# Kernel tuning notes

Hardware: AMD Instinct MI355X
Metric: run time of the kernel (lower is better)

Reference implementation:

```python
import jax, jax.numpy as jnp
import numpy as np

AZ = -999999.0  # ALMOST_ZERO_LOG_SCALE
N = 100000      # nodes
E = N - 1       # tree edges
D = 768         # input_dim
H = 256         # hidden_dim
C = 16          # num_classes


def setup_inputs() -> dict:
    key = jax.random.key(0)
    ks = jax.random.split(key, 14)
    scale = 0.02
    features = jax.random.normal(ks[0], (N, D), dtype=jnp.float32)
    # tree edges: child i (1..N-1) has parent sampled from [0, N)
    parent_idx = jax.random.randint(ks[1], (E,), 0, N, dtype=jnp.int32)
    child_idx = jnp.arange(1, N, dtype=jnp.int32)
    label_observed = jax.random.randint(ks[2], (N,), 0, 2, dtype=jnp.int32)
    true_labels = jax.random.randint(ks[3], (N,), 0, C, dtype=jnp.int32)
    # MLP feature extractor (num_layers=2, Linear+ReLU each, feature_extractor=True)
    W1 = jax.random.normal(ks[4], (D, H), dtype=jnp.float32) * scale
    b1 = jnp.zeros((H,), dtype=jnp.float32)
    W2 = jax.random.normal(ks[5], (H, H), dtype=jnp.float32) * scale
    b2 = jnp.zeros((H,), dtype=jnp.float32)
    # build_unary_potentials: Linear(H, C)
    Wu = jax.random.normal(ks[6], (H, C), dtype=jnp.float32) * scale
    bu = jnp.zeros((C,), dtype=jnp.float32)
    # build_edge_potentials: Linear(2H, C*C)
    We = jax.random.normal(ks[7], (2 * H, C * C), dtype=jnp.float32) * scale
    be = jnp.zeros((C * C,), dtype=jnp.float32)
    return {
        "features": features, "parent_idx": parent_idx, "child_idx": child_idx,
        "label_observed": label_observed, "true_labels": true_labels,
        "W1": W1, "b1": b1, "W2": W2, "b2": b2,
        "Wu": Wu, "bu": bu, "We": We, "be": be,
    }


def reference(features, parent_idx, child_idx, label_observed, true_labels,
              W1, b1, W2, b2, Wu, bu, We, be):
    obs = label_observed.astype(bool)
    # MLP feature extractor over all nodes at once (original loops per-node)
    h = jax.nn.relu(features @ W1 + b1)
    h = jax.nn.relu(h @ W2 + b2)                      # [N, H]
    # unary potentials; observed nodes get 0 at true label, AZ elsewhere
    unary_pred = h @ Wu + bu                          # [N, C]
    lbl = jnp.arange(C, dtype=true_labels.dtype)
    obs_unary = jnp.where(true_labels[:, None] == lbl[None, :], 0.0, AZ)
    unary = jnp.where(obs[:, None], obs_unary, unary_pred)  # [N, C]
    # edge potentials: Linear on concat(parent_hidden, child_hidden)
    hp = h[parent_idx]                                # [E, H]
    hc = h[child_idx]                                 # [E, H]
    ep = (jnp.concatenate([hp, hc], axis=1) @ We + be).reshape(E, C, C)
    pl = true_labels[parent_idx]                      # [E]
    cl = true_labels[child_idx]                       # [E]
    op = obs[parent_idx]                              # [E]
    oc = obs[child_idx]                               # [E]
    row = lbl[None, :, None]                          # broadcast over rows
    col = lbl[None, None, :]                          # broadcast over cols
    # both observed: 0 at [parent_label, child_label], AZ elsewhere
    allow_both = (row == pl[:, None, None]) & (col == cl[:, None, None])
    both = (op & oc)[:, None, None]
    # child-only observed: keep row at child label; parent-only: keep col at parent label
    keep = (((oc & ~op)[:, None, None] & (row == cl[:, None, None]))
            | ((op & ~oc)[:, None, None] & (col == pl[:, None, None]))
            | (~op & ~oc)[:, None, None])
    ep_masked = jnp.where(both,
                          jnp.where(allow_both, 0.0, AZ),
                          jnp.where(keep, ep, ep + AZ))
    return unary, ep_masked
```

## Files before the change

kernel.cpp:

```cpp
#include <hip/hip_runtime.h>
#include <cstddef>

#define AZ -999999.0f

typedef float  f32x4  __attribute__((ext_vector_type(4)));
typedef short  s16x8  __attribute__((ext_vector_type(8)));
typedef __bf16 bf16x8 __attribute__((ext_vector_type(8)));
typedef unsigned short ushort_t;

__device__ __forceinline__ ushort_t f2bf(float f) {
    return __builtin_bit_cast(ushort_t, (__bf16)f);
}

__device__ __forceinline__ f32x4 mfma16(s16x8 a, s16x8 b, f32x4 c) {
    return __builtin_amdgcn_mfma_f32_16x16x32_bf16(
        __builtin_bit_cast(bf16x8, a), __builtin_bit_cast(bf16x8, b), c, 0, 0, 0);
}

__device__ __forceinline__ void gl2lds16(const void* g, void* l) {
    __builtin_amdgcn_global_load_lds(
        (const __attribute__((address_space(1))) unsigned int*)g,
        (__attribute__((address_space(3))) unsigned int*)l, 16, 0, 0);
}

#define FENCE() asm volatile("" ::: "memory")

__global__ void setup_kernel(
    const float* __restrict__ W1, const float* __restrict__ W2,
    const float* __restrict__ We, const float* __restrict__ Wu,
    ushort_t* __restrict__ W1T, ushort_t* __restrict__ W2T,
    ushort_t* __restrict__ WeT, ushort_t* __restrict__ WuTs,
    const int* __restrict__ pidx, const int* __restrict__ cidx,
    const int* __restrict__ tl, const int* __restrict__ obs,
    int* __restrict__ meta, int E)
{
    int b = blockIdx.x, t = threadIdx.x;
    if (b < 768) {
        int idx = b * 256 + t; int k = idx >> 8, n = idx & 255;
        W1T[(size_t)n * 768 + k] = f2bf(W1[idx]);
    } else if (b < 1024) {
        int idx = (b - 768) * 256 + t; int k = idx >> 8, n = idx & 255;
        W2T[n * 256 + k] = f2bf(W2[idx]);
    } else if (b < 1536) {
        int idx = (b - 1024) * 256 + t; int k = idx >> 8, n = idx & 255;
        WeT[(size_t)n * 512 + k] = f2bf(We[idx]);
    } else if (b < 1552) {
        int idx = (b - 1536) * 256 + t; int k = idx >> 4, c = idx & 15;
        WuTs[c * 256 + (((k >> 3) ^ (c & 7)) << 3) + (k & 7)] = f2bf(Wu[idx]);
    } else {
        int e = (b - 1552) * 256 + t;
        if (e < E) {
            int p = pidx[e], c = cidx[e];
            meta[e] = (tl[p] & 15) | ((tl[c] & 15) << 4)
                    | ((obs[p] & 1) << 8) | ((obs[c] & 1) << 9);
        }
    }
}

__global__ __launch_bounds__(256) void node_fused_kernel(
    const float* __restrict__ features, const ushort_t* __restrict__ W1T,
    const float* __restrict__ b1, const ushort_t* __restrict__ W2T,
    const float* __restrict__ b2, const ushort_t* __restrict__ WuTs,
    const float* __restrict__ bu, const int* __restrict__ tl,
    const int* __restrict__ obs, ushort_t* __restrict__ h2,
    float* __restrict__ out_unary, int N)
{
    __shared__ __align__(16) char smem[49152];
    ushort_t* Hsh = (ushort_t*)smem;

    const int tid = threadIdx.x, lane = tid & 63, wave = tid >> 6;
    const int quad = lane >> 4, l16 = lane & 15;
    const int row0 = blockIdx.x * 64;
    const int wc = wave * 64;

    const int c4 = tid & 3, rB = tid >> 2;
    const int gcB = c4 ^ ((rB >> 1) & 3);
    unsigned lds_b[4]; size_t b1_off[4];
#pragma unroll
    for (int j = 0; j < 4; ++j) {
        lds_b[j]  = (unsigned)(j * 64 + wave * 16) * 64;
        b1_off[j] = (size_t)(j * 64 + rB) * 768 + gcB * 8;
    }

    const int c8 = tid & 7, r8 = tid >> 3;
    const int gcA = c8 ^ (r8 & 7);
    size_t a_off[2]; unsigned lds_a[2];
#pragma unroll
    for (int j = 0; j < 2; ++j) {
        int gr = row0 + j * 32 + r8; if (gr > N - 1) gr = N - 1;
        a_off[j] = (size_t)gr * 768 + gcA * 4;
        lds_a[j] = (unsigned)(j * 32 + wave * 8) * 128;
    }

    const f32x4 fz = {0.f, 0.f, 0.f, 0.f};
    f32x4 acc[4][4];
#pragma unroll
    for (int i = 0; i < 4; ++i)
#pragma unroll
        for (int j = 0; j < 4; ++j) acc[i][j] = fz;

    auto stageA = [&](int kt, int b) {
        const int kbase = kt << 5;
        char* Ab = smem + b * 8192;
#pragma unroll
        for (int j = 0; j < 2; ++j)
            gl2lds16(features + a_off[j] + kbase, Ab + lds_a[j]);
    };
    auto stageB1 = [&](int kt, int b) {
        const int kbase = kt << 5;
        char* Bb = smem + 16384 + b * 16384;
#pragma unroll
        for (int j = 0; j < 4; ++j)
            gl2lds16(W1T + b1_off[j] + kbase, Bb + lds_b[j]);
    };
    auto stageB2 = [&](int kt) {
        const int kbase = kt << 5;
        char* Bb = smem + 32768;
#pragma unroll
        for (int j = 0; j < 4; ++j)
            gl2lds16(W2T + (size_t)(j * 64 + rB) * 256 + gcB * 8 + kbase,
                     Bb + lds_b[j]);
    };

    stageA(0, 0); stageB1(0, 0);
    int cur = 0;
    for (int kt = 0; kt < 24; ++kt) {
        if (kt < 23) {
            stageA(kt + 1, cur ^ 1); stageB1(kt + 1, cur ^ 1);
            asm volatile("s_waitcnt vmcnt(6)" ::: "memory");
        } else {
            asm volatile("s_waitcnt vmcnt(0)" ::: "memory");
        }
        __builtin_amdgcn_s_barrier();
        FENCE();

        const float*    Asf = (const float*)(smem + cur * 8192);
        const ushort_t* Bsh = (const ushort_t*)(smem + 16384 + cur * 16384);
        s16x8 af[4], bf[4];
        const int s = l16 & 7;
        const int c0 = (2 * quad) ^ s, c1 = c0 ^ 1;
#pragma unroll
        for (int f = 0; f < 4; ++f) {
            int row = f * 16 + l16;
            f32x4 v0 = *(const f32x4*)&Asf[row * 32 + c0 * 4];
            f32x4 v1 = *(const f32x4*)&Asf[row * 32 + c1 * 4];
            s16x8 a;
            a[0] = (short)f2bf(v0[0]); a[1] = (short)f2bf(v0[1]);
            a[2] = (short)f2bf(v0[2]); a[3] = (short)f2bf(v0[3]);
            a[4] = (short)f2bf(v1[0]); a[5] = (short)f2bf(v1[1]);
            a[6] = (short)f2bf(v1[2]); a[7] = (short)f2bf(v1[3]);
            af[f] = a;
        }
        const int cb = quad ^ ((l16 >> 1) & 3);
#pragma unroll
        for (int f = 0; f < 4; ++f)
            bf[f] = *(const s16x8*)&Bsh[(wc + f * 16 + l16) * 32 + cb * 8];
#pragma unroll
        for (int fr = 0; fr < 4; ++fr)
#pragma unroll
            for (int fc = 0; fc < 4; ++fc)
                acc[fr][fc] = mfma16(af[fr], bf[fc], acc[fr][fc]);

        FENCE();
        __builtin_amdgcn_s_barrier();
        cur ^= 1;
    }
    stageB2(0);

    {
        float bv[4];
#pragma unroll
        for (int fc = 0; fc < 4; ++fc) bv[fc] = b1[wc + fc * 16 + l16];
#pragma unroll
        for (int fr = 0; fr < 4; ++fr) {
#pragma unroll
            for (int r = 0; r < 4; ++r) {
                int row = fr * 16 + quad * 4 + r;
#pragma unroll
                for (int fc = 0; fc < 4; ++fc) {
                    int col = wc + fc * 16 + l16;
                    float v = acc[fr][fc][r] + bv[fc];
                    v = v > 0.f ? v : 0.f;
                    Hsh[row * 256 + (((col >> 3) ^ (row & 7)) << 3) + (col & 7)] = f2bf(v);
                }
            }
        }
    }
#pragma unroll
    for (int i = 0; i < 4; ++i)
#pragma unroll
        for (int j = 0; j < 4; ++j) acc[i][j] = fz;

    asm volatile("s_waitcnt lgkmcnt(0)" ::: "memory");
    __builtin_amdgcn_s_barrier();
    FENCE();

    for (int kt = 0; kt < 8; ++kt) {
        asm volatile("s_waitcnt vmcnt(0)" ::: "memory");
        __builtin_amdgcn_s_barrier();
        FENCE();

        const ushort_t* Bsh = (const ushort_t*)(smem + 32768);
        s16x8 af[4], bf[4];
        const int pc = (kt * 4 + quad) ^ (l16 & 7);
#pragma unroll
        for (int f = 0; f < 4; ++f)
            af[f] = *(const s16x8*)&Hsh[(f * 16 + l16) * 256 + pc * 8];
        const int cb = quad ^ ((l16 >> 1) & 3);
#pragma unroll
        for (int f = 0; f < 4; ++f)
            bf[f] = *(const s16x8*)&Bsh[(wc + f * 16 + l16) * 32 + cb * 8];
#pragma unroll
        for (int fr = 0; fr < 4; ++fr)
#pragma unroll
            for (int fc = 0; fc < 4; ++fc)
                acc[fr][fc] = mfma16(af[fr], bf[fc], acc[fr][fc]);

        FENCE();
        __builtin_amdgcn_s_barrier();
        if (kt < 7) stageB2(kt + 1);
    }

    {
        float bv[4];
#pragma unroll
        for (int fc = 0; fc < 4; ++fc) bv[fc] = b2[wc + fc * 16 + l16];
#pragma unroll
        for (int fr = 0; fr < 4; ++fr) {
#pragma unroll
            for (int r = 0; r < 4; ++r) {
                int row = fr * 16 + quad * 4 + r;
#pragma unroll
                for (int fc = 0; fc < 4; ++fc) {
                    int col = wc + fc * 16 + l16;
                    float v = acc[fr][fc][r] + bv[fc];
                    v = v > 0.f ? v : 0.f;
                    Hsh[row * 256 + (((col >> 3) ^ (row & 7)) << 3) + (col & 7)] = f2bf(v);
                }
            }
        }
    }
    asm volatile("s_waitcnt lgkmcnt(0)" ::: "memory");
    __builtin_amdgcn_s_barrier();
    FENCE();

    {
        int row = tid >> 2, cc = tid & 3;
        int gr = row0 + row;
        if (gr < N) {
#pragma unroll
            for (int j = 0; j < 8; ++j) {
                int phys = (j * 4 + cc) ^ (row & 7);
                s16x8 v = *(const s16x8*)&Hsh[row * 256 + phys * 8];
                *(s16x8*)&h2[(size_t)gr * 256 + (j * 4 + cc) * 8] = v;
            }
        }
    }

    {
        const int arow = wave * 16 + l16;
        f32x4 accu = fz;
#pragma unroll
        for (int kt = 0; kt < 8; ++kt) {
            int pc = (kt * 4 + quad) ^ (l16 & 7);
            s16x8 a = *(const s16x8*)&Hsh[arow * 256 + pc * 8];
            s16x8 b = *(const s16x8*)&WuTs[l16 * 256 + pc * 8];
            accu = mfma16(a, b, accu);
        }
        float bvc = bu[l16];
#pragma unroll
        for (int r = 0; r < 4; ++r) {
            int node = row0 + wave * 16 + quad * 4 + r;
            if (node < N) {
                float v = obs[node] ? ((tl[node] == l16) ? 0.0f : AZ) : (accu[r] + bvc);
                out_unary[(size_t)node * 16 + l16] = v;
            }
        }
    }
}

__global__ __launch_bounds__(256) void edge_gemm_kernel(
    const ushort_t* __restrict__ h2, const ushort_t* __restrict__ WeT,
    const float* __restrict__ bias, float* __restrict__ out,
    int M,
    const int* __restrict__ parent_idx, const int* __restrict__ child_idx,
    const int* __restrict__ meta)
{
    __shared__ __align__(16) char smem[40960];

    const int tid  = threadIdx.x;
    const int lane = tid & 63, wave = tid >> 6;
    const int row0 = blockIdx.x * 64;
    const int wc   = wave * 64;
    const int quad = lane >> 4, l16 = lane & 15;
    const int c4   = tid & 3, rB = tid >> 2;

    const int gcB = c4 ^ ((rB >> 1) & 3);
    size_t   b_off[4]; unsigned lds_b[4];
#pragma unroll
    for (int j = 0; j < 4; ++j) {
        b_off[j] = (size_t)(j * 64 + rB) * 512 + gcB * 8;
        lds_b[j] = (unsigned)(j * 64 + wave * 16) * 64;
    }

    int gr = row0 + rB; if (gr > M - 1) gr = M - 1;
    const int pn = parent_idx[gr], cn = child_idx[gr];
    const unsigned a_col  = (unsigned)gcB * 8;
    const unsigned lds_a0 = (unsigned)(wave * 16) * 64;

    auto stage = [&](int kt, int b) {
        const int kbase = kt << 5;
        int node = (kbase < 256) ? pn : cn;
        gl2lds16(h2 + (size_t)node * 256 + (kbase & 255) + a_col,
                 smem + b * 4096 + lds_a0);
#pragma unroll
        for (int j = 0; j < 4; ++j)
            gl2lds16(WeT + b_off[j] + kbase,
                     smem + 8192 + b * 16384 + lds_b[j]);
    };

    const f32x4 fz = {0.f, 0.f, 0.f, 0.f};
    f32x4 acc[4][4];
#pragma unroll
    for (int i = 0; i < 4; ++i)
#pragma unroll
        for (int j = 0; j < 4; ++j) acc[i][j] = fz;

    stage(0, 0);
    int cur = 0;
    for (int kt = 0; kt < 16; ++kt) {
        if (kt < 15) {
            stage(kt + 1, cur ^ 1);
            asm volatile("s_waitcnt vmcnt(5)" ::: "memory");
        } else {
            asm volatile("s_waitcnt vmcnt(0)" ::: "memory");
        }
        __builtin_amdgcn_s_barrier();
        FENCE();

        const ushort_t* Ash = (const ushort_t*)(smem + cur * 4096);
        const ushort_t* Bsh = (const ushort_t*)(smem + 8192 + cur * 16384);
        s16x8 af[4], bf[4];
        const int ca = quad ^ ((l16 >> 1) & 3);
#pragma unroll
        for (int f = 0; f < 4; ++f)
            af[f] = *(const s16x8*)&Ash[(f * 16 + l16) * 32 + ca * 8];
#pragma unroll
        for (int f = 0; f < 4; ++f)
            bf[f] = *(const s16x8*)&Bsh[(wc + f * 16 + l16) * 32 + ca * 8];
#pragma unroll
        for (int fr = 0; fr < 4; ++fr)
#pragma unroll
            for (int fc = 0; fc < 4; ++fc)
                acc[fr][fc] = mfma16(af[fr], bf[fc], acc[fr][fc]);

        FENCE();
        __builtin_amdgcn_s_barrier();
        cur ^= 1;
    }

    float bv[4];
#pragma unroll
    for (int fc = 0; fc < 4; ++fc) bv[fc] = bias[wc + fc * 16 + l16];

#pragma unroll
    for (int fr = 0; fr < 4; ++fr) {
#pragma unroll
        for (int r = 0; r < 4; ++r) {
            int e = row0 + fr * 16 + quad * 4 + r;
            if (e < M) {
                int m  = meta[e];
                int pl = m & 15, cl = (m >> 4) & 15;
                int op = (m >> 8) & 1, oc = (m >> 9) & 1;
#pragma unroll
                for (int fc = 0; fc < 4; ++fc) {
                    int n = wc + fc * 16 + l16;
                    float v = acc[fr][fc][r] + bv[fc];
                    int rr = n >> 4, cc = n & 15;
                    if (op & oc)  v = (rr == pl && cc == cl) ? 0.0f : AZ;
                    else if (oc)  { if (rr != cl) v += AZ; }
                    else if (op)  { if (cc != pl) v += AZ; }
                    out[(size_t)e * 256 + n] = v;
                }
            }
        }
    }
}

extern "C" void kernel_launch(void* const* d_in, const int* in_sizes, int n_in,
                              void* d_out, int out_size, void* d_ws, size_t ws_size,
                              hipStream_t stream) {
    const float* features = (const float*)d_in[0];
    const int* parent_idx = (const int*)d_in[1];
    const int* child_idx  = (const int*)d_in[2];
    const int* label_obs  = (const int*)d_in[3];
    const int* true_lab   = (const int*)d_in[4];
    const float* W1 = (const float*)d_in[5];
    const float* b1 = (const float*)d_in[6];
    const float* W2 = (const float*)d_in[7];
    const float* b2 = (const float*)d_in[8];
    const float* Wu = (const float*)d_in[9];
    const float* bu = (const float*)d_in[10];
    const float* We = (const float*)d_in[11];
    const float* be = (const float*)d_in[12];
    float* out = (float*)d_out;

    const int N = 100000, E = N - 1;

    char* ws = (char*)d_ws;
    ushort_t* h2   = (ushort_t*)ws;
    ushort_t* W1T  = (ushort_t*)(ws + (size_t)N * 256 * 2);
    ushort_t* W2T  = W1T + 768 * 256;
    ushort_t* WeT  = W2T + 256 * 256;
    ushort_t* WuTs = WeT + 512 * 256;
    int*      meta = (int*)(WuTs + 16 * 256);

    setup_kernel<<<1943, 256, 0, stream>>>(W1, W2, We, Wu, W1T, W2T, WeT, WuTs,
                                           parent_idx, child_idx, true_lab, label_obs,
                                           meta, E);

    node_fused_kernel<<<(N + 63) / 64, 256, 0, stream>>>(
        features, W1T, b1, W2T, b2, WuTs, bu, true_lab, label_obs, h2, out, N);

    edge_gemm_kernel<<<(E + 63) / 64, 256, 0, stream>>>(
        h2, WeT, be, out + (size_t)N * 16, E, parent_idx, child_idx, meta);
}
```

Before: 578.8 us.

## Load weight B-fragments directly from global into registers, shrinking LDS

In both the node MLP and the edge GEMM kernels, the weight tiles (W1T, W2T, WeT) are no longer staged through LDS. Each wave now loads its MFMA B fragments straight from global memory into registers, double-buffered with explicit register sets, while only the activation A tiles stay in LDS. This cuts LDS use (48KB to 32KB, 40KB to 8KB) to allow more resident blocks, and removes LDS traffic and barriers for the second-layer weights. The cost is that each wave now issues its own global loads for weights, relying on L2/L1 hits, and register pressure goes up.

```diff
diff --git a/kernel.cpp b/kernel.cpp
--- a/kernel.cpp
+++ b/kernel.cpp
@@ -65,7 +65,7 @@
     const int* __restrict__ obs, ushort_t* __restrict__ h2,
     float* __restrict__ out_unary, int N)
 {
-    __shared__ __align__(16) char smem[49152];
+    __shared__ __align__(16) char smem[32768];
     ushort_t* Hsh = (ushort_t*)smem;
 
     const int tid = threadIdx.x, lane = tid & 63, wave = tid >> 6;
@@ -73,15 +73,6 @@
     const int row0 = blockIdx.x * 64;
     const int wc = wave * 64;
 
-    const int c4 = tid & 3, rB = tid >> 2;
-    const int gcB = c4 ^ ((rB >> 1) & 3);
-    unsigned lds_b[4]; size_t b1_off[4];
-#pragma unroll
-    for (int j = 0; j < 4; ++j) {
-        lds_b[j]  = (unsigned)(j * 64 + wave * 16) * 64;
-        b1_off[j] = (size_t)(j * 64 + rB) * 768 + gcB * 8;
-    }
-
     const int c8 = tid & 7, r8 = tid >> 3;
     const int gcA = c8 ^ (r8 & 7);
     size_t a_off[2]; unsigned lds_a[2];
@@ -92,6 +83,14 @@
         lds_a[j] = (unsigned)(j * 32 + wave * 8) * 128;
     }
 
+    unsigned b1o[4], b2o[4];
+#pragma unroll
+    for (int f = 0; f < 4; ++f) {
+        int row = wc + f * 16 + l16;
+        b1o[f] = (unsigned)row * 768 + quad * 8;
+        b2o[f] = (unsigned)row * 256 + quad * 8;
+    }
+
     const f32x4 fz = {0.f, 0.f, 0.f, 0.f};
     f32x4 acc[4][4];
 #pragma unroll
@@ -106,37 +105,9 @@
         for (int j = 0; j < 2; ++j)
             gl2lds16(features + a_off[j] + kbase, Ab + lds_a[j]);
     };
-    auto stageB1 = [&](int kt, int b) {
-        const int kbase = kt << 5;
-        char* Bb = smem + 16384 + b * 16384;
-#pragma unroll
-        for (int j = 0; j < 4; ++j)
-            gl2lds16(W1T + b1_off[j] + kbase, Bb + lds_b[j]);
-    };
-    auto stageB2 = [&](int kt) {
-        const int kbase = kt << 5;
-        char* Bb = smem + 32768;
-#pragma unroll
-        for (int j = 0; j < 4; ++j)
-            gl2lds16(W2T + (size_t)(j * 64 + rB) * 256 + gcB * 8 + kbase,
-                     Bb + lds_b[j]);
-    };
-
-    stageA(0, 0); stageB1(0, 0);
-    int cur = 0;
-    for (int kt = 0; kt < 24; ++kt) {
-        if (kt < 23) {
-            stageA(kt + 1, cur ^ 1); stageB1(kt + 1, cur ^ 1);
-            asm volatile("s_waitcnt vmcnt(6)" ::: "memory");
-        } else {
-            asm volatile("s_waitcnt vmcnt(0)" ::: "memory");
-        }
-        __builtin_amdgcn_s_barrier();
-        FENCE();
-
-        const float*    Asf = (const float*)(smem + cur * 8192);
-        const ushort_t* Bsh = (const ushort_t*)(smem + 16384 + cur * 16384);
-        s16x8 af[4], bf[4];
+
+    auto compute1 = [&](const float* Asf, const s16x8* bf) {
+        s16x8 af[4];
         const int s = l16 & 7;
         const int c0 = (2 * quad) ^ s, c1 = c0 ^ 1;
 #pragma unroll
@@ -151,21 +122,47 @@
             a[6] = (short)f2bf(v1[2]); a[7] = (short)f2bf(v1[3]);
             af[f] = a;
         }
-        const int cb = quad ^ ((l16 >> 1) & 3);
-#pragma unroll
-        for (int f = 0; f < 4; ++f)
-            bf[f] = *(const s16x8*)&Bsh[(wc + f * 16 + l16) * 32 + cb * 8];
 #pragma unroll
         for (int fr = 0; fr < 4; ++fr)
 #pragma unroll
             for (int fc = 0; fc < 4; ++fc)
                 acc[fr][fc] = mfma16(af[fr], bf[fc], acc[fr][fc]);
-
-        FENCE();
-        __builtin_amdgcn_s_barrier();
-        cur ^= 1;
-    }
-    stageB2(0);
+    };
+
+    stageA(0, 0);
+    s16x8 bA[4], bB[4];
+#pragma unroll
+    for (int f = 0; f < 4; ++f) bA[f] = *(const s16x8*)(W1T + b1o[f]);
+
+    for (int t = 0; t < 12; ++t) {
+        const int kt0 = 2 * t, kt1 = kt0 + 1;
+        stageA(kt0 + 1, 1);
+        {
+            const int ko = (kt0 + 1) << 5;
+#pragma unroll
+            for (int f = 0; f < 4; ++f) bB[f] = *(const s16x8*)(W1T + b1o[f] + ko);
+        }
+        asm volatile("s_waitcnt vmcnt(6)" ::: "memory");
+        __builtin_amdgcn_s_barrier();
+        FENCE();
+        compute1((const float*)smem, bA);
+        FENCE();
+        __builtin_amdgcn_s_barrier();
+        if (kt1 < 23) {
+            stageA(kt1 + 1, 0);
+            const int ko = (kt1 + 1) << 5;
+#pragma unroll
+            for (int f = 0; f < 4; ++f) bA[f] = *(const s16x8*)(W1T + b1o[f] + ko);
+            asm volatile("s_waitcnt vmcnt(6)" ::: "memory");
+        } else {
+            asm volatile("s_waitcnt vmcnt(0)" ::: "memory");
+        }
+        __builtin_amdgcn_s_barrier();
+        FENCE();
+        compute1((const float*)(smem + 8192), bB);
+        FENCE();
+        __builtin_amdgcn_s_barrier();
+    }
 
     {
         float bv[4];
@@ -195,31 +192,27 @@
     __builtin_amdgcn_s_barrier();
     FENCE();
 
+#pragma unroll 2
     for (int kt = 0; kt < 8; ++kt) {
-        asm volatile("s_waitcnt vmcnt(0)" ::: "memory");
-        __builtin_amdgcn_s_barrier();
-        FENCE();
-
-        const ushort_t* Bsh = (const ushort_t*)(smem + 32768);
+        const int pc = (kt * 4 + quad) ^ (l16 & 7);
+        const int ko = kt << 5;
         s16x8 af[4], bf[4];
-        const int pc = (kt * 4 + quad) ^ (l16 & 7);
 #pragma unroll
         for (int f = 0; f < 4; ++f)
             af[f] = *(const s16x8*)&Hsh[(f * 16 + l16) * 256 + pc * 8];
-        const int cb = quad ^ ((l16 >> 1) & 3);
 #pragma unroll
         for (int f = 0; f < 4; ++f)
-            bf[f] = *(const s16x8*)&Bsh[(wc + f * 16 + l16) * 32 + cb * 8];
+            bf[f] = *(const s16x8*)(W2T + b2o[f] + ko);
 #pragma unroll
         for (int fr = 0; fr < 4; ++fr)
 #pragma unroll
             for (int fc = 0; fc < 4; ++fc)
                 acc[fr][fc] = mfma16(af[fr], bf[fc], acc[fr][fc]);
-
-        FENCE();
-        __builtin_amdgcn_s_barrier();
-        if (kt < 7) stageB2(kt + 1);
-    }
+    }
+
+    FENCE();
+    __builtin_amdgcn_s_barrier();
+    FENCE();
 
     {
         float bv[4];
@@ -286,37 +279,31 @@
     const int* __restrict__ parent_idx, const int* __restrict__ child_idx,
     const int* __restrict__ meta)
 {
-    __shared__ __align__(16) char smem[40960];
+    __shared__ __align__(16) char smem[8192];
 
     const int tid  = threadIdx.x;
     const int lane = tid & 63, wave = tid >> 6;
     const int row0 = blockIdx.x * 64;
     const int wc   = wave * 64;
     const int quad = lane >> 4, l16 = lane & 15;
-    const int c4   = tid & 3, rB = tid >> 2;
-
-    const int gcB = c4 ^ ((rB >> 1) & 3);
-    size_t   b_off[4]; unsigned lds_b[4];
-#pragma unroll
-    for (int j = 0; j < 4; ++j) {
-        b_off[j] = (size_t)(j * 64 + rB) * 512 + gcB * 8;
-        lds_b[j] = (unsigned)(j * 64 + wave * 16) * 64;
-    }
-
-    int gr = row0 + rB; if (gr > M - 1) gr = M - 1;
+    const int c4   = tid & 3, rA = tid >> 2;
+
+    const int gsw = c4 ^ ((rA >> 1) & 3);
+    int gr = row0 + rA; if (gr > M - 1) gr = M - 1;
     const int pn = parent_idx[gr], cn = child_idx[gr];
-    const unsigned a_col  = (unsigned)gcB * 8;
+    const unsigned a_col  = (unsigned)gsw * 8;
     const unsigned lds_a0 = (unsigned)(wave * 16) * 64;
 
-    auto stage = [&](int kt, int b) {
+    unsigned beo[4];
+#pragma unroll
+    for (int f = 0; f < 4; ++f)
+        beo[f] = (unsigned)(wc + f * 16 + l16) * 512 + quad * 8;
+
+    auto stageA = [&](int kt, int b) {
         const int kbase = kt << 5;
-        int node = (kbase < 256) ? pn : cn;
+        int node = (kt < 8) ? pn : cn;
         gl2lds16(h2 + (size_t)node * 256 + (kbase & 255) + a_col,
                  smem + b * 4096 + lds_a0);
-#pragma unroll
-        for (int j = 0; j < 4; ++j)
-            gl2lds16(WeT + b_off[j] + kbase,
-                     smem + 8192 + b * 16384 + lds_b[j]);
     };
 
     const f32x4 fz = {0.f, 0.f, 0.f, 0.f};
@@ -326,37 +313,52 @@
 #pragma unroll
         for (int j = 0; j < 4; ++j) acc[i][j] = fz;
 
-    stage(0, 0);
-    int cur = 0;
-    for (int kt = 0; kt < 16; ++kt) {
-        if (kt < 15) {
-            stage(kt + 1, cur ^ 1);
+    auto computeE = [&](const ushort_t* Ash, const s16x8* bf) {
+        s16x8 af[4];
+        const int ca = quad ^ ((l16 >> 1) & 3);
+#pragma unroll
+        for (int f = 0; f < 4; ++f)
+            af[f] = *(const s16x8*)&Ash[(f * 16 + l16) * 32 + ca * 8];
+#pragma unroll
+        for (int fr = 0; fr < 4; ++fr)
+#pragma unroll
+            for (int fc = 0; fc < 4; ++fc)
+                acc[fr][fc] = mfma16(af[fr], bf[fc], acc[fr][fc]);
+    };
+
+    stageA(0, 0);
+    s16x8 bA[4], bB[4];
+#pragma unroll
+    for (int f = 0; f < 4; ++f) bA[f] = *(const s16x8*)(WeT + beo[f]);
+
+    for (int t = 0; t < 8; ++t) {
+        const int kt0 = 2 * t, kt1 = kt0 + 1;
+        stageA(kt0 + 1, 1);
+        {
+            const int ko = (kt0 + 1) << 5;
+#pragma unroll
+            for (int f = 0; f < 4; ++f) bB[f] = *(const s16x8*)(WeT + beo[f] + ko);
+        }
+        asm volatile("s_waitcnt vmcnt(5)" ::: "memory");
+        __builtin_amdgcn_s_barrier();
+        FENCE();
+        computeE((const ushort_t*)smem, bA);
+        FENCE();
+        __builtin_amdgcn_s_barrier();
+        if (kt1 < 15) {
+            stageA(kt1 + 1, 0);
+            const int ko = (kt1 + 1) << 5;
+#pragma unroll
+            for (int f = 0; f < 4; ++f) bA[f] = *(const s16x8*)(WeT + beo[f] + ko);
             asm volatile("s_waitcnt vmcnt(5)" ::: "memory");
         } else {
             asm volatile("s_waitcnt vmcnt(0)" ::: "memory");
         }
         __builtin_amdgcn_s_barrier();
         FENCE();
-
-        const ushort_t* Ash = (const ushort_t*)(smem + cur * 4096);
-        const ushort_t* Bsh = (const ushort_t*)(smem + 8192 + cur * 16384);
-        s16x8 af[4], bf[4];
-        const int ca = quad ^ ((l16 >> 1) & 3);
-#pragma unroll
-        for (int f = 0; f < 4; ++f)
-            af[f] = *(const s16x8*)&Ash[(f * 16 + l16) * 32 + ca * 8];
-#pragma unroll
-        for (int f = 0; f < 4; ++f)
-            bf[f] = *(const s16x8*)&Bsh[(wc + f * 16 + l16) * 32 + ca * 8];
-#pragma unroll
-        for (int fr = 0; fr < 4; ++fr)
-#pragma unroll
-            for (int fc = 0; fc < 4; ++fc)
-                acc[fr][fc] = mfma16(af[fr], bf[fc], acc[fr][fc]);
-
-        FENCE();
-        __builtin_amdgcn_s_barrier();
-        cur ^= 1;
+        computeE((const ushort_t*)(smem + 4096), bB);
+        FENCE();
+        __builtin_amdgcn_s_barrier();
     }
 
     float bv[4];
```

Measured after the change: 646.7 us. +11.7%, slower.
